# Performance work log

Hardware: AMD Instinct MI355X
Metric: run time of the kernel (lower is better)

## Reference

```python
import jax, jax.numpy as jnp
import numpy as np

Q_BITS = 8
GELU_A = -0.2888
GELU_B = -1.769
INV_SQRT2 = 0.7071067811865476


def _ste_round(x):
    # straight-through round (identity grad)
    return x + jax.lax.stop_gradient(jnp.round(x) - x)


def fake_quant_weight(w):
    # per-tensor symmetric int8 fake quant
    qmax = 2.0 ** (Q_BITS - 1) - 1.0  # 127
    s = jnp.maximum(jnp.max(jnp.abs(w)), 1e-8) / qmax
    q = jnp.clip(_ste_round(w / s), -qmax - 1.0, qmax)
    return q * s


def fake_quant_act(x):
    # per-tensor asymmetric uint8 fake quant
    levels = 2.0 ** Q_BITS - 1.0  # 255
    xmin = jax.lax.stop_gradient(jnp.min(x))
    xmax = jax.lax.stop_gradient(jnp.max(x))
    s = jnp.maximum(xmax - xmin, 1e-8) / levels
    zp = jnp.round(-xmin / s)
    q = jnp.clip(_ste_round(x / s) + zp, 0.0, levels)
    return (q - zp) * s


def int_gelu(x):
    # I-BERT polynomial GELU: gelu(x) = x * 0.5 * (1 + L(x/sqrt(2)))
    # L(t) = sign(t) * (a * (clip(|t|, 0, -b) + b)^2 + 1)
    t = x * INV_SQRT2
    at = jnp.minimum(jnp.abs(t), -GELU_B)
    L = jnp.sign(t) * (GELU_A * (at + GELU_B) ** 2 + 1.0)
    return x * 0.5 * (1.0 + L)


def setup_inputs() -> dict:
    key = jax.random.key(0)
    k = jax.random.split(key, 5)
    B, S, D, H = 64, 197, 768, 3072
    x = jax.random.normal(k[0], (B, S, D), dtype=jnp.float32)
    w1 = jax.random.normal(k[1], (H, D), dtype=jnp.float32) * (1.0 / np.sqrt(D))
    b1 = jax.random.normal(k[2], (H,), dtype=jnp.float32) * 0.02
    w2 = jax.random.normal(k[3], (D, H), dtype=jnp.float32) * (1.0 / np.sqrt(H))
    b2 = jax.random.normal(k[4], (D,), dtype=jnp.float32) * 0.02
    return {"x": x, "w1": w1, "b1": b1, "w2": w2, "b2": b2}


def reference(x, w1, b1, w2, b2):
    # QuantLinear 1: fake-quant act + weight, then GEMM
    xq = fake_quant_act(x)
    h = jnp.einsum('bsd,hd->bsh', xq, fake_quant_weight(w1)) + b1
    # IntGELU (dropout is identity in eval)
    g = int_gelu(h)
    # QuantLinear 2
    gq = fake_quant_act(g)
    out = jnp.einsum('bsh,dh->bsd', gq, fake_quant_weight(w2)) + b2
    return out
```

## Files before the change

kernel.cpp:

```cpp
#include <hip/hip_runtime.h>
#include <stdint.h>
#include <stddef.h>

typedef int v4i  __attribute__((ext_vector_type(4)));
typedef int v16i __attribute__((ext_vector_type(16)));

#define GELU_A   (-0.2888f)
#define GELU_B   (-1.769f)
#define INV_SQRT2 0.70710678118654752440f

#define GLD16(gp, lp) __builtin_amdgcn_global_load_lds( \
    (const __attribute__((address_space(1))) unsigned int*)(gp), \
    (__attribute__((address_space(3))) unsigned int*)(lp), 16, 0, 0)

#define WAIT_VM4 0x0F74
#define WAIT_VM0 0x0F70

__device__ __forceinline__ unsigned enc_f(float f){
  unsigned u = __float_as_uint(f);
  return (u & 0x80000000u) ? ~u : (u | 0x80000000u);
}
__device__ __forceinline__ float dec_f(unsigned e){
  unsigned u = (e & 0x80000000u) ? (e & 0x7FFFFFFFu) : ~e;
  return __uint_as_float(u);
}

__device__ __forceinline__ float int_gelu_f(float x){
  float t = x * INV_SQRT2;
  float at = fminf(fabsf(t), 1.769f);
  float u = at + GELU_B;
  float p = GELU_A * (u * u) + 1.0f;
  float L = (t > 0.0f) ? p : ((t < 0.0f) ? -p : 0.0f);
  return x * 0.5f * (1.0f + L);
}

__global__ void init_scalars(unsigned* sc){
  if (threadIdx.x == 0){
    sc[0] = 0xFFFFFFFFu;
    sc[1] = 0u;
    sc[2] = 0u;
    sc[3] = 0u;
    sc[4] = 0xFFFFFFFFu;
    sc[5] = 0u;
  }
}

__global__ __launch_bounds__(256) void reduce_stats(
    const float4* __restrict__ x, int nx4,
    const float4* __restrict__ w1, int n14,
    const float4* __restrict__ w2, int n24,
    unsigned* __restrict__ sc)
{
  __shared__ float ra[256], rb[256];
  const int tid = threadIdx.x;
  const int b = blockIdx.x;
  if (b < 1024){
    float lmin = 3.4e38f, lmax = -3.4e38f;
    for (long i = (long)b * 256 + tid; i < nx4; i += 1024L * 256L){
      float4 v = x[i];
      lmin = fminf(lmin, fminf(fminf(v.x, v.y), fminf(v.z, v.w)));
      lmax = fmaxf(lmax, fmaxf(fmaxf(v.x, v.y), fmaxf(v.z, v.w)));
    }
    ra[tid] = lmin; rb[tid] = lmax;
    __syncthreads();
    for (int s = 128; s > 0; s >>= 1){
      if (tid < s){ ra[tid] = fminf(ra[tid], ra[tid + s]); rb[tid] = fmaxf(rb[tid], rb[tid + s]); }
      __syncthreads();
    }
    if (tid == 0){
      atomicMin(&sc[0], enc_f(ra[0]));
      atomicMax(&sc[1], enc_f(rb[0]));
    }
  } else {
    const float4* w; int n4; int slot; int bl;
    if (b < 1152){ w = w1; n4 = n14; slot = 2; bl = b - 1024; }
    else         { w = w2; n4 = n24; slot = 3; bl = b - 1152; }
    float la = 0.0f;
    for (long i = (long)bl * 256 + tid; i < n4; i += 128L * 256L){
      float4 v = w[i];
      la = fmaxf(la, fmaxf(fmaxf(fabsf(v.x), fabsf(v.y)), fmaxf(fabsf(v.z), fabsf(v.w))));
    }
    ra[tid] = la;
    __syncthreads();
    for (int s = 128; s > 0; s >>= 1){
      if (tid < s) ra[tid] = fmaxf(ra[tid], ra[tid + s]);
      __syncthreads();
    }
    if (tid == 0) atomicMax(&sc[slot], __float_as_uint(ra[0]));
  }
}

__global__ __launch_bounds__(256) void quant_act(
    const float4* __restrict__ in, unsigned* __restrict__ out, long n4,
    const unsigned* __restrict__ sc, int slot)
{
  const float vmin = dec_f(sc[slot]);
  const float vmax = dec_f(sc[slot + 1]);
  const float s  = fmaxf(vmax - vmin, 1e-8f) / 255.0f;
  const float zp = rintf(-vmin / s);
  const long stride = (long)gridDim.x * blockDim.x;
  for (long i = (long)blockIdx.x * blockDim.x + threadIdx.x; i < n4; i += stride){
    float4 v = in[i];
    int q0 = (int)fminf(fmaxf(rintf(v.x / s) + zp, 0.0f), 255.0f) - 128;
    int q1 = (int)fminf(fmaxf(rintf(v.y / s) + zp, 0.0f), 255.0f) - 128;
    int q2 = (int)fminf(fmaxf(rintf(v.z / s) + zp, 0.0f), 255.0f) - 128;
    int q3 = (int)fminf(fmaxf(rintf(v.w / s) + zp, 0.0f), 255.0f) - 128;
    out[i] = ((unsigned)(q0 & 255)) | ((unsigned)(q1 & 255) << 8) |
             ((unsigned)(q2 & 255) << 16) | ((unsigned)(q3 & 255) << 24);
  }
}

__global__ __launch_bounds__(256) void quant_w(
    const float* __restrict__ w1, const float* __restrict__ w2,
    int8_t* __restrict__ qw1, int8_t* __restrict__ qw2,
    int* __restrict__ rs1, int* __restrict__ rs2,
    const unsigned* __restrict__ sc, int n1, int k1, int k2)
{
  __shared__ int red[256];
  const int b = blockIdx.x, tid = threadIdx.x;
  const float* w; int8_t* q; int* rs; int K; int n; float s;
  if (b < n1){ w = w1; q = qw1; rs = rs1; K = k1; n = b;
               s = fmaxf(__uint_as_float(sc[2]), 1e-8f) / 127.0f; }
  else       { w = w2; q = qw2; rs = rs2; K = k2; n = b - n1;
               s = fmaxf(__uint_as_float(sc[3]), 1e-8f) / 127.0f; }
  int sum = 0;
  for (int k = tid; k < K; k += 256){
    float v = w[(size_t)n * K + k];
    float qf = fminf(fmaxf(rintf(v / s), -128.0f), 127.0f);
    int qi = (int)qf;
    q[(size_t)n * K + k] = (int8_t)qi;
    sum += qi;
  }
  red[tid] = sum;
  __syncthreads();
  for (int st = 128; st > 0; st >>= 1){
    if (tid < st) red[tid] += red[tid + st];
    __syncthreads();
  }
  if (tid == 0) rs[n] = red[0];
}

template<int MODE>
__global__ __launch_bounds__(256) void gemm_i8(
    const int8_t* __restrict__ A, const int8_t* __restrict__ Bm,
    const int* __restrict__ rowsum, const float* __restrict__ bias,
    void* __restrict__ Cout, int M, int N, int K,
    unsigned* __restrict__ sc)
{
  __shared__ __align__(16) int8_t lds[3][16384];

  const int tid  = threadIdx.x;
  const int lane = tid & 63;
  const int wave = tid >> 6;
  const int l31  = lane & 31;
  const int kh   = lane >> 5;
  const int n0   = blockIdx.x * 128;
  const int m0   = blockIdx.y * 128;
  const int wm   = (wave & 1) * 64;
  const int wn   = (wave >> 1) * 64;

  int aoffs[2], boffs[2];
  const int ldst[2] = { wave * 2048, wave * 2048 + 1024 };
#pragma unroll
  for (int t = 0; t < 2; t++){
    int rowl = wave * 32 + t * 16 + (lane >> 2);
    int csw  = ((lane & 3) ^ ((rowl >> 1) & 3)) << 4;
    int ga = m0 + rowl; if (ga >= M) ga = M - 1;
    aoffs[t] = ga * K + csw;
    boffs[t] = (n0 + rowl) * K + csw;
  }

  const int w2  = (l31 >> 1) & 3;
  const int sA0 = (kh ^ w2) << 4;
  int arow[2], brow[2];
#pragma unroll
  for (int mi = 0; mi < 2; mi++){
    arow[mi] = (wm + mi * 32 + l31) * 64;
    brow[mi] = (wn + mi * 32 + l31) * 64;
  }

  v16i acc[2][2] = {};
  const int NT = K >> 6;

#pragma unroll
  for (int t = 0; t < 2; t++){
    GLD16(A  + aoffs[t],      &lds[0][ldst[t]]);
    GLD16(Bm + boffs[t],      &lds[0][8192 + ldst[t]]);
  }
#pragma unroll
  for (int t = 0; t < 2; t++){
    GLD16(A  + aoffs[t] + 64, &lds[1][ldst[t]]);
    GLD16(Bm + boffs[t] + 64, &lds[1][8192 + ldst[t]]);
  }

  for (int kt = 0; kt < NT; kt++){
    const int8_t* buf = lds[kt % 3];
    if (kt + 1 < NT) __builtin_amdgcn_s_waitcnt(WAIT_VM4);
    else             __builtin_amdgcn_s_waitcnt(WAIT_VM0);
    __builtin_amdgcn_s_barrier();
    __builtin_amdgcn_sched_barrier(0);

    v4i af[2][2], bf[2][2];
#pragma unroll
    for (int kk = 0; kk < 2; kk++){
      const int sb = sA0 ^ (kk << 5);
#pragma unroll
      for (int mi = 0; mi < 2; mi++){
        af[kk][mi] = *(const v4i*)(buf + arow[mi] + sb);
        bf[kk][mi] = *(const v4i*)(buf + 8192 + brow[mi] + sb);
      }
    }

    if (kt + 2 < NT){
      int8_t* nbuf = lds[(kt + 2) % 3];
      const int ko = (kt + 2) << 6;
#pragma unroll
      for (int t = 0; t < 2; t++){
        GLD16(A  + aoffs[t] + ko, nbuf + ldst[t]);
        GLD16(Bm + boffs[t] + ko, nbuf + 8192 + ldst[t]);
      }
    }

#pragma unroll
    for (int kk = 0; kk < 2; kk++)
#pragma unroll
      for (int mi = 0; mi < 2; mi++)
#pragma unroll
        for (int nj = 0; nj < 2; nj++)
          acc[mi][nj] = __builtin_amdgcn_mfma_i32_32x32x32_i8(af[kk][mi], bf[kk][nj], acc[mi][nj], 0, 0, 0);
  }

  float s_h, off_h;
  if constexpr (MODE == 1){
    float gmin = dec_f(sc[4]), gmax = dec_f(sc[5]);
    float sg = fmaxf(gmax - gmin, 1e-8f) / 255.0f;
    float zp = rintf(-gmin / sg);
    float sw = fmaxf(__uint_as_float(sc[3]), 1e-8f) / 127.0f;
    s_h = sg * sw; off_h = 128.0f - zp;
  } else {
    float xmin = dec_f(sc[0]), xmax = dec_f(sc[1]);
    float sx = fmaxf(xmax - xmin, 1e-8f) / 255.0f;
    float zp = rintf(-xmin / sx);
    float sw = fmaxf(__uint_as_float(sc[2]), 1e-8f) / 127.0f;
    s_h = sx * sw; off_h = 128.0f - zp;
  }
  float qs = 1.0f, qzp = 0.0f;
  if constexpr (MODE == 2){
    float gmin = dec_f(sc[4]), gmax = dec_f(sc[5]);
    qs = fmaxf(gmax - gmin, 1e-8f) / 255.0f;
    qzp = rintf(-gmin / qs);
  }

  float lmin = 3.4e38f, lmax = -3.4e38f;
#pragma unroll
  for (int nj = 0; nj < 2; nj++){
    const int n = n0 + wn + nj * 32 + l31;
    const float rsv = off_h * (float)rowsum[n];
    const float bv = bias[n];
#pragma unroll
    for (int mi = 0; mi < 2; mi++){
      const int mbase = m0 + wm + mi * 32 + 4 * kh;
#pragma unroll
      for (int r = 0; r < 16; r++){
        const int m = mbase + (r & 3) + 8 * (r >> 2);
        if (m < M){
          float h = s_h * ((float)acc[mi][nj][r] + rsv) + bv;
          if constexpr (MODE == 0){
            float gv = int_gelu_f(h);
            lmin = fminf(lmin, gv); lmax = fmaxf(lmax, gv);
          } else if constexpr (MODE == 2){
            float gv = int_gelu_f(h);
            float qf = fminf(fmaxf(rintf(gv / qs) + qzp, 0.0f), 255.0f);
            ((int8_t*)Cout)[(size_t)m * N + n] = (int8_t)((int)qf - 128);
          } else {
            ((float*)Cout)[(size_t)m * N + n] = h;
          }
        }
      }
    }
  }

  if constexpr (MODE == 0){
    __syncthreads();
    float* redA = (float*)&lds[0][0];
    float* redB = ((float*)&lds[0][0]) + 256;
    redA[tid] = lmin; redB[tid] = lmax;
    __syncthreads();
    for (int st = 128; st > 0; st >>= 1){
      if (tid < st){
        redA[tid] = fminf(redA[tid], redA[tid + st]);
        redB[tid] = fmaxf(redB[tid], redB[tid + st]);
      }
      __syncthreads();
    }
    if (tid == 0){
      atomicMin(&sc[4], enc_f(redA[0]));
      atomicMax(&sc[5], enc_f(redB[0]));
    }
  }
}

extern "C" void kernel_launch(void* const* d_in, const int* in_sizes, int n_in,
                              void* d_out, int out_size, void* d_ws, size_t ws_size,
                              hipStream_t stream)
{
  const float* x  = (const float*)d_in[0];
  const float* w1 = (const float*)d_in[1];
  const float* b1 = (const float*)d_in[2];
  const float* w2 = (const float*)d_in[3];
  const float* b2 = (const float*)d_in[4];
  float* out = (float*)d_out;

  const int H = in_sizes[2];
  const int D = in_sizes[4];
  const int M = in_sizes[0] / D;

  char* ws = (char*)d_ws;
  unsigned* sc = (unsigned*)ws;
  size_t off = 256;
  int8_t* qx  = (int8_t*)(ws + off); off += (size_t)M * D;
  int8_t* qw1 = (int8_t*)(ws + off); off += (size_t)H * D;
  int8_t* qw2 = (int8_t*)(ws + off); off += (size_t)D * H;
  int* rs1 = (int*)(ws + off); off += (size_t)H * 4;
  int* rs2 = (int*)(ws + off); off += 4096;
  int8_t* qg  = (int8_t*)(ws + off); off += (size_t)M * H;
  (void)ws_size; (void)n_in; (void)out_size;

  init_scalars<<<dim3(1), dim3(64), 0, stream>>>(sc);

  reduce_stats<<<dim3(1280), dim3(256), 0, stream>>>(
      (const float4*)x, M * D / 4,
      (const float4*)w1, H * D / 4,
      (const float4*)w2, D * H / 4, sc);

  quant_act<<<dim3(2048), dim3(256), 0, stream>>>(
      (const float4*)x, (unsigned*)qx, (long)M * D / 4, sc, 0);

  quant_w<<<dim3(H + D), dim3(256), 0, stream>>>(
      w1, w2, qw1, qw2, rs1, rs2, sc, H, D, H);

  gemm_i8<0><<<dim3(H / 128, (M + 127) / 128), dim3(256), 0, stream>>>(
      qx, qw1, rs1, b1, nullptr, M, H, D, sc);

  gemm_i8<2><<<dim3(H / 128, (M + 127) / 128), dim3(256), 0, stream>>>(
      qx, qw1, rs1, b1, qg, M, H, D, sc);

  gemm_i8<1><<<dim3(D / 128, (M + 127) / 128), dim3(256), 0, stream>>>(
      qg, qw2, rs2, b2, out, M, D, H, sc);
}
```

Baseline: 354.0 us.

## Store GELU output as fp16 to avoid recomputing first GEMM, fuse quant kernels

The first GEMM previously ran twice, once to find the GELU min/max and once to quantize. The new path runs it once and stores GELU output as fp16 in the workspace, then a separate quantization kernel converts it to int8 using the global stats. The activation and weight quantization kernels are merged into one launch, and the init kernel is replaced by memsets with the scalar slots reordered. This trades one int8 GEMM for an fp16 write and read of M*H elements, plus possible fp16 rounding differences near quantization boundaries.

```diff
diff --git a/kernel.cpp b/kernel.cpp
--- a/kernel.cpp
+++ b/kernel.cpp
@@ -4,6 +4,7 @@
 
 typedef int v4i  __attribute__((ext_vector_type(4)));
 typedef int v16i __attribute__((ext_vector_type(16)));
+typedef _Float16 vh8 __attribute__((ext_vector_type(8)));
 
 #define GELU_A   (-0.2888f)
 #define GELU_B   (-1.769f)
@@ -15,6 +16,7 @@
 
 #define WAIT_VM4 0x0F74
 #define WAIT_VM0 0x0F70
+
 
 __device__ __forceinline__ unsigned enc_f(float f){
   unsigned u = __float_as_uint(f);
@@ -32,17 +34,6 @@
   float p = GELU_A * (u * u) + 1.0f;
   float L = (t > 0.0f) ? p : ((t < 0.0f) ? -p : 0.0f);
   return x * 0.5f * (1.0f + L);
-}
-
-__global__ void init_scalars(unsigned* sc){
-  if (threadIdx.x == 0){
-    sc[0] = 0xFFFFFFFFu;
-    sc[1] = 0u;
-    sc[2] = 0u;
-    sc[3] = 0u;
-    sc[4] = 0xFFFFFFFFu;
-    sc[5] = 0u;
-  }
 }
 
 __global__ __launch_bounds__(256) void reduce_stats(
@@ -69,12 +60,12 @@
     }
     if (tid == 0){
       atomicMin(&sc[0], enc_f(ra[0]));
-      atomicMax(&sc[1], enc_f(rb[0]));
+      atomicMax(&sc[2], enc_f(rb[0]));
     }
   } else {
     const float4* w; int n4; int slot; int bl;
-    if (b < 1152){ w = w1; n4 = n14; slot = 2; bl = b - 1024; }
-    else         { w = w2; n4 = n24; slot = 3; bl = b - 1152; }
+    if (b < 1152){ w = w1; n4 = n14; slot = 3; bl = b - 1024; }
+    else         { w = w2; n4 = n24; slot = 4; bl = b - 1152; }
     float la = 0.0f;
     for (long i = (long)bl * 256 + tid; i < n4; i += 128L * 256L){
       float4 v = w[i];
@@ -90,54 +81,79 @@
   }
 }
 
-__global__ __launch_bounds__(256) void quant_act(
-    const float4* __restrict__ in, unsigned* __restrict__ out, long n4,
-    const unsigned* __restrict__ sc, int slot)
-{
-  const float vmin = dec_f(sc[slot]);
-  const float vmax = dec_f(sc[slot + 1]);
-  const float s  = fmaxf(vmax - vmin, 1e-8f) / 255.0f;
-  const float zp = rintf(-vmin / s);
-  const long stride = (long)gridDim.x * blockDim.x;
-  for (long i = (long)blockIdx.x * blockDim.x + threadIdx.x; i < n4; i += stride){
-    float4 v = in[i];
-    int q0 = (int)fminf(fmaxf(rintf(v.x / s) + zp, 0.0f), 255.0f) - 128;
-    int q1 = (int)fminf(fmaxf(rintf(v.y / s) + zp, 0.0f), 255.0f) - 128;
-    int q2 = (int)fminf(fmaxf(rintf(v.z / s) + zp, 0.0f), 255.0f) - 128;
-    int q3 = (int)fminf(fmaxf(rintf(v.w / s) + zp, 0.0f), 255.0f) - 128;
-    out[i] = ((unsigned)(q0 & 255)) | ((unsigned)(q1 & 255) << 8) |
-             ((unsigned)(q2 & 255) << 16) | ((unsigned)(q3 & 255) << 24);
-  }
-}
-
-__global__ __launch_bounds__(256) void quant_w(
+__global__ __launch_bounds__(256) void quant_all(
+    const float4* __restrict__ x, unsigned* __restrict__ qx, long nx4,
     const float* __restrict__ w1, const float* __restrict__ w2,
     int8_t* __restrict__ qw1, int8_t* __restrict__ qw2,
     int* __restrict__ rs1, int* __restrict__ rs2,
-    const unsigned* __restrict__ sc, int n1, int k1, int k2)
-{
-  __shared__ int red[256];
-  const int b = blockIdx.x, tid = threadIdx.x;
-  const float* w; int8_t* q; int* rs; int K; int n; float s;
-  if (b < n1){ w = w1; q = qw1; rs = rs1; K = k1; n = b;
-               s = fmaxf(__uint_as_float(sc[2]), 1e-8f) / 127.0f; }
-  else       { w = w2; q = qw2; rs = rs2; K = k2; n = b - n1;
-               s = fmaxf(__uint_as_float(sc[3]), 1e-8f) / 127.0f; }
-  int sum = 0;
-  for (int k = tid; k < K; k += 256){
-    float v = w[(size_t)n * K + k];
-    float qf = fminf(fmaxf(rintf(v / s), -128.0f), 127.0f);
-    int qi = (int)qf;
-    q[(size_t)n * K + k] = (int8_t)qi;
-    sum += qi;
-  }
-  red[tid] = sum;
-  __syncthreads();
-  for (int st = 128; st > 0; st >>= 1){
-    if (tid < st) red[tid] += red[tid + st];
-    __syncthreads();
-  }
-  if (tid == 0) rs[n] = red[0];
+    const unsigned* __restrict__ sc, int H, int D)
+{
+  const int tid = threadIdx.x;
+  const int b = blockIdx.x;
+  if (b < 2048){
+    const float vmin = dec_f(sc[0]);
+    const float vmax = dec_f(sc[2]);
+    const float s  = fmaxf(vmax - vmin, 1e-8f) / 255.0f;
+    const float zp = rintf(-vmin / s);
+    for (long i = (long)b * 256 + tid; i < nx4; i += 2048L * 256L){
+      float4 v = x[i];
+      int q0 = (int)fminf(fmaxf(rintf(v.x / s) + zp, 0.0f), 255.0f) - 128;
+      int q1 = (int)fminf(fmaxf(rintf(v.y / s) + zp, 0.0f), 255.0f) - 128;
+      int q2 = (int)fminf(fmaxf(rintf(v.z / s) + zp, 0.0f), 255.0f) - 128;
+      int q3 = (int)fminf(fmaxf(rintf(v.w / s) + zp, 0.0f), 255.0f) - 128;
+      qx[i] = ((unsigned)(q0 & 255)) | ((unsigned)(q1 & 255) << 8) |
+              ((unsigned)(q2 & 255) << 16) | ((unsigned)(q3 & 255) << 24);
+    }
+  } else {
+    __shared__ int red[256];
+    const int wb = b - 2048;
+    const float* w; int8_t* q; int* rs; int K; int n; float s;
+    if (wb < H){ w = w1; q = qw1; rs = rs1; K = D; n = wb;
+                 s = fmaxf(__uint_as_float(sc[3]), 1e-8f) / 127.0f; }
+    else       { w = w2; q = qw2; rs = rs2; K = H; n = wb - H;
+                 s = fmaxf(__uint_as_float(sc[4]), 1e-8f) / 127.0f; }
+    int sum = 0;
+    for (int k = tid; k < K; k += 256){
+      float v = w[(size_t)n * K + k];
+      float qf = fminf(fmaxf(rintf(v / s), -128.0f), 127.0f);
+      int qi = (int)qf;
+      q[(size_t)n * K + k] = (int8_t)qi;
+      sum += qi;
+    }
+    red[tid] = sum;
+    __syncthreads();
+    for (int st = 128; st > 0; st >>= 1){
+      if (tid < st) red[tid] += red[tid + st];
+      __syncthreads();
+    }
+    if (tid == 0) rs[n] = red[0];
+  }
+}
+
+__global__ __launch_bounds__(256) void quant_g(
+    const vh8* __restrict__ g, uint2* __restrict__ qg, long n8,
+    const unsigned* __restrict__ sc)
+{
+  const float gmin = dec_f(sc[1]), gmax = dec_f(sc[5]);
+  const float qs  = fmaxf(gmax - gmin, 1e-8f) / 255.0f;
+  const float qzp = rintf(-gmin / qs);
+  const long stride = (long)gridDim.x * blockDim.x;
+  for (long i = (long)blockIdx.x * blockDim.x + threadIdx.x; i < n8; i += stride){
+    vh8 v = g[i];
+    unsigned lo = 0, hi = 0;
+#pragma unroll
+    for (int j = 0; j < 4; j++){
+      int q = (int)fminf(fmaxf(rintf((float)v[j] / qs) + qzp, 0.0f), 255.0f) - 128;
+      lo |= ((unsigned)(q & 255)) << (8 * j);
+    }
+#pragma unroll
+    for (int j = 0; j < 4; j++){
+      int q = (int)fminf(fmaxf(rintf((float)v[4 + j] / qs) + qzp, 0.0f), 255.0f) - 128;
+      hi |= ((unsigned)(q & 255)) << (8 * j);
+    }
+    uint2 o; o.x = lo; o.y = hi;
+    qg[i] = o;
+  }
 }
 
 template<int MODE>
@@ -232,21 +248,21 @@
 
   float s_h, off_h;
   if constexpr (MODE == 1){
-    float gmin = dec_f(sc[4]), gmax = dec_f(sc[5]);
+    float gmin = dec_f(sc[1]), gmax = dec_f(sc[5]);
     float sg = fmaxf(gmax - gmin, 1e-8f) / 255.0f;
     float zp = rintf(-gmin / sg);
-    float sw = fmaxf(__uint_as_float(sc[3]), 1e-8f) / 127.0f;
+    float sw = fmaxf(__uint_as_float(sc[4]), 1e-8f) / 127.0f;
     s_h = sg * sw; off_h = 128.0f - zp;
   } else {
-    float xmin = dec_f(sc[0]), xmax = dec_f(sc[1]);
+    float xmin = dec_f(sc[0]), xmax = dec_f(sc[2]);
     float sx = fmaxf(xmax - xmin, 1e-8f) / 255.0f;
     float zp = rintf(-xmin / sx);
-    float sw = fmaxf(__uint_as_float(sc[2]), 1e-8f) / 127.0f;
+    float sw = fmaxf(__uint_as_float(sc[3]), 1e-8f) / 127.0f;
     s_h = sx * sw; off_h = 128.0f - zp;
   }
   float qs = 1.0f, qzp = 0.0f;
   if constexpr (MODE == 2){
-    float gmin = dec_f(sc[4]), gmax = dec_f(sc[5]);
+    float gmin = dec_f(sc[1]), gmax = dec_f(sc[5]);
     qs = fmaxf(gmax - gmin, 1e-8f) / 255.0f;
     qzp = rintf(-gmin / qs);
   }
@@ -268,6 +284,10 @@
           if constexpr (MODE == 0){
             float gv = int_gelu_f(h);
             lmin = fminf(lmin, gv); lmax = fmaxf(lmax, gv);
+          } else if constexpr (MODE == 3){
+            float gv = int_gelu_f(h);
+            lmin = fminf(lmin, gv); lmax = fmaxf(lmax, gv);
+            ((_Float16*)Cout)[(size_t)m * N + n] = (_Float16)gv;
           } else if constexpr (MODE == 2){
             float gv = int_gelu_f(h);
             float qf = fminf(fmaxf(rintf(gv / qs) + qzp, 0.0f), 255.0f);
@@ -280,7 +300,7 @@
     }
   }
 
-  if constexpr (MODE == 0){
+  if constexpr (MODE == 0 || MODE == 3){
     __syncthreads();
     float* redA = (float*)&lds[0][0];
     float* redB = ((float*)&lds[0][0]) + 256;
@@ -294,7 +314,7 @@
       __syncthreads();
     }
     if (tid == 0){
-      atomicMin(&sc[4], enc_f(redA[0]));
+      atomicMin(&sc[1], enc_f(redA[0]));
       atomicMax(&sc[5], enc_f(redB[0]));
     }
   }
@@ -324,27 +344,32 @@
   int* rs1 = (int*)(ws + off); off += (size_t)H * 4;
   int* rs2 = (int*)(ws + off); off += 4096;
   int8_t* qg  = (int8_t*)(ws + off); off += (size_t)M * H;
-  (void)ws_size; (void)n_in; (void)out_size;
-
-  init_scalars<<<dim3(1), dim3(64), 0, stream>>>(sc);
+  _Float16* g16 = (_Float16*)(ws + off);
+  const size_t need_big = off + (size_t)M * H * 2;
+  (void)n_in; (void)out_size;
+
+  hipMemsetAsync(sc, 0xFF, 8, stream);
+  hipMemsetAsync(sc + 2, 0x00, 16, stream);
 
   reduce_stats<<<dim3(1280), dim3(256), 0, stream>>>(
       (const float4*)x, M * D / 4,
       (const float4*)w1, H * D / 4,
       (const float4*)w2, D * H / 4, sc);
 
-  quant_act<<<dim3(2048), dim3(256), 0, stream>>>(
-      (const float4*)x, (unsigned*)qx, (long)M * D / 4, sc, 0);
-
-  quant_w<<<dim3(H + D), dim3(256), 0, stream>>>(
-      w1, w2, qw1, qw2, rs1, rs2, sc, H, D, H);
-
-  gemm_i8<0><<<dim3(H / 128, (M + 127) / 128), dim3(256), 0, stream>>>(
-      qx, qw1, rs1, b1, nullptr, M, H, D, sc);
-
-  gemm_i8<2><<<dim3(H / 128, (M + 127) / 128), dim3(256), 0, stream>>>(
-      qx, qw1, rs1, b1, qg, M, H, D, sc);
-
-  gemm_i8<1><<<dim3(D / 128, (M + 127) / 128), dim3(256), 0, stream>>>(
-      qg, qw2, rs2, b2, out, M, D, H, sc);
-}
+  quant_all<<<dim3(2048 + H + D), dim3(256), 0, stream>>>(
+      (const float4*)x, (unsigned*)qx, (long)M * D / 4,
+      w1, w2, qw1, qw2, rs1, rs2, sc, H, D);
+
+  const dim3 g1(H / 128, (M + 127) / 128), g2(D / 128, (M + 127) / 128), blk(256);
+
+  if (ws_size >= need_big){
+    gemm_i8<3><<<g1, blk, 0, stream>>>(qx, qw1, rs1, b1, g16, M, H, D, sc);
+    quant_g<<<dim3(2048), blk, 0, stream>>>(
+        (const vh8*)g16, (uint2*)qg, (long)M * H / 8, sc);
+  } else {
+    gemm_i8<0><<<g1, blk, 0, stream>>>(qx, qw1, rs1, b1, nullptr, M, H, D, sc);
+    gemm_i8<2><<<g1, blk, 0, stream>>>(qx, qw1, rs1, b1, qg, M, H, D, sc);
+  }
+
+  gemm_i8<1><<<g2, blk, 0, stream>>>(qg, qw2, rs2, b2, out, M, D, H, sc);
+}
```

New measurement: 308.9 us. 12.7% less time.
